# Optimization experiments

Measured on AMD Instinct MI355X. Metric: run time of the kernel, lower is better.

The kernel has to match this reference:

```python
import jax, jax.numpy as jnp
import numpy as np

B, CIN, COUT, T = 64, 2048, 2048, 128
BLOCK = 8            # structured-sparsity block size from _create_structured_sparse_mask
SPARSITY = 0.9       # keep probability per block = 1 - SPARSITY
SPIKE_PROB = 0.1     # binary input spike rate


def setup_inputs() -> dict:
    key = jax.random.key(0)
    k1, k2, k3 = jax.random.split(key, 3)
    # binary input spikes [B, Cin, T] (torch casts to int8; values are 0/1)
    spikes = (jax.random.uniform(k1, (B, CIN, T)) < SPIKE_PROB).astype(jnp.float32)
    # int8 quantized weights held as float32 (values in [-127,127))
    weights = jax.random.randint(k2, (COUT, CIN), -127, 127).astype(jnp.float32)
    # block-structured sparse connectivity mask, block 8x8, keep prob 0.1
    keep = jax.random.uniform(k3, (COUT // BLOCK, CIN // BLOCK)) > SPARSITY
    mask = jnp.repeat(jnp.repeat(keep, BLOCK, axis=0), BLOCK, axis=1).astype(jnp.float32)
    scale_exp = jnp.zeros((COUT,), dtype=jnp.int32)  # weight_scale_exp init zeros
    return {"spikes": spikes, "weights": weights, "mask": mask,
            "scale_exp": scale_exp, "threshold_exp": 7}


def reference(spikes, weights, mask, scale_exp, threshold_exp):
    # spikes: [B, Cin, T]; weights/mask: [Cout, Cin]; scale_exp: [Cout]
    masked_w = weights * mask                              # [Cout, Cin]
    scale = jnp.exp2(scale_exp.astype(jnp.float32))        # 2**weight_scale_exp per channel
    thr = jnp.float32(2.0) ** threshold_exp                # 2**threshold_exp (=128)
    s_t = jnp.transpose(spikes, (2, 0, 1))                 # [T, B, Cin]
    acc0 = jnp.zeros((spikes.shape[0], weights.shape[0]), jnp.float32)

    def step(acc, st):
        # integrate: sparse-masked matmul + power-of-two per-channel scale
        acc = acc + (st @ masked_w.T) * scale              # [B, Cout]
        spk = (acc >= thr).astype(jnp.float32)             # fire
        acc = acc * (1.0 - spk)                            # reset fired neurons to 0
        return acc, spk

    _, out = jax.lax.scan(step, acc0, s_t)                 # out: [T, B, Cout]
    return jnp.transpose(out, (1, 2, 0))                   # [B, Cout, T]
```

## Files before the change

kernel.cpp:

```cpp
#include <hip/hip_runtime.h>

#define BB   64
#define CIN  2048
#define COUT 2048
#define TT   128

#define NPAIR 64
#define NWIN  4
#define SLOTW 32
#define BC_CAP 7680

typedef int i32x4 __attribute__((ext_vector_type(4)));

__device__ __forceinline__ void async16(char* lds_dst, const char* g_src) {
    __builtin_amdgcn_global_load_lds(
        (const __attribute__((address_space(1))) void*)g_src,
        (__attribute__((address_space(3))) void*)lds_dst,
        16, 0, 0);
}

__global__ void prep1(const float* __restrict__ spikes,
                      const float* __restrict__ msk,
                      char* __restrict__ A,
                      unsigned long long* __restrict__ kb) {
    int bid = blockIdx.x;
    int tid = threadIdx.x;

    if (bid >= 8192) {
        int rb = bid - 8192;
        bool keep = (msk[(size_t)(rb * 8) * CIN + tid * 8] != 0.f);
        unsigned long long m = __ballot(keep);
        if ((tid & 63) == 0) kb[rb * 4 + (tid >> 6)] = m;
        return;
    }

    __shared__ float tile[64][33];
    int cc = bid & 31;
    int tt = (bid >> 5) & 3;
    int b  = bid >> 7;
    int c0 = cc * 64, t0 = tt * 32;

    int t4 = tid & 7;
    int cr = tid >> 3;
#pragma unroll
    for (int s = 0; s < 2; ++s) {
        int c = cr + s * 32;
        float4 v = *(const float4*)(spikes + ((size_t)b * CIN + c0 + c) * TT + t0 + t4 * 4);
        tile[c][t4 * 4 + 0] = v.x;
        tile[c][t4 * 4 + 1] = v.y;
        tile[c][t4 * 4 + 2] = v.z;
        tile[c][t4 * 4 + 3] = v.w;
    }
    __syncthreads();

    int tw_ = tid >> 4;
    int cq  = tid & 15;
#pragma unroll
    for (int s2 = 0; s2 < 2; ++s2) {
        int tw = tw_ + s2 * 16;
        int packed = 0;
#pragma unroll
        for (int q = 0; q < 4; ++q)
            packed |= ((tile[cq * 4 + q][tw] != 0.f) ? 1 : 0) << (8 * q);
        *(int*)(A + ((size_t)(b * TT) + t0 + tw) * CIN + c0 + cq * 4) = packed;
    }
}

__global__ void prep2(const float* __restrict__ w,
                      const float* __restrict__ msk,
                      const unsigned long long* __restrict__ kb,
                      char* __restrict__ Bc,
                      unsigned short* __restrict__ lst,
                      unsigned* __restrict__ ofs_g,
                      unsigned* __restrict__ nch_g) {
    __shared__ unsigned sbm[256];
    __shared__ unsigned snch[256];
    __shared__ unsigned sofs[256];
    const int tid = threadIdx.x;
    const int pw_self = blockIdx.x;

    {
        int p = tid >> 2, wdw = tid & 3;
        unsigned long long r = kb[(4 * p + 0) * 4 + wdw] | kb[(4 * p + 1) * 4 + wdw] |
                               kb[(4 * p + 2) * 4 + wdw] | kb[(4 * p + 3) * 4 + wdw];
        unsigned long long t2 = r | (r >> 1);
        unsigned bm = 0u;
#pragma unroll
        for (int s = 0; s < 32; ++s)
            bm |= (unsigned)((t2 >> (2 * s)) & 1ull) << s;
        sbm[tid]  = bm;
        snch[tid] = (unsigned)((__popc(bm) + 3) >> 2);
    }
    __syncthreads();
    if (tid == 0) {
        unsigned run = 0;
#pragma unroll 4
        for (int i = 0; i < 256; ++i) { sofs[i] = run; run += snch[i] * 4; }
        ofs_g[pw_self] = sofs[pw_self];
        nch_g[pw_self] = snch[pw_self];
    }
    __syncthreads();

    const int p = pw_self >> 2, wdw = pw_self & 3;
    unsigned rem = sbm[pw_self];
    const unsigned o = sofs[pw_self];
    const unsigned nslots = snch[pw_self] * 4;

    for (unsigned j = 0; j < nslots; ++j) {
        int kl = 0;
        bool real = false;
        if (rem) { kl = __ffs(rem) - 1; rem &= rem - 1u; real = true; }
        int kk = wdw * SLOTW + kl;
        if (tid < 128) {
            int col = tid >> 2, q = tid & 3;
            unsigned pk = 0u;
            if (real) {
                size_t base = (size_t)(p * 32 + col) * CIN + kk * 16 + q * 4;
                float4 a = *(const float4*)(w + base);
                float4 m = *(const float4*)(msk + base);
                int b0 = (int)(char)(int)(a.x * m.x);
                int b1 = (int)(char)(int)(a.y * m.y);
                int b2 = (int)(char)(int)(a.z * m.z);
                int b3 = (int)(char)(int)(a.w * m.w);
                pk = (unsigned)((b0 & 0xFF) | ((b1 & 0xFF) << 8) | ((b2 & 0xFF) << 16) | (b3 << 24));
            }
            *(unsigned*)(Bc + (size_t)(o + j) * 512 + col * 16 + q * 4) = pk;
        }
        if (tid == 0) lst[o + j] = (unsigned short)(real ? kl : 0);
    }
}

__global__ void __launch_bounds__(512, 4)
snn_gemm_scan(const char* __restrict__ A,
              const char* __restrict__ Bc,
              const unsigned short* __restrict__ lst,
              const unsigned* __restrict__ ofs,
              const unsigned* __restrict__ nchv,
              const int* __restrict__ scale_exp,
              const int* __restrict__ thr_exp,
              float* __restrict__ out) {
    __shared__ __align__(16) union {
        struct {
            char a[128 * 512];
            unsigned short l[8 * SLOTW];
            unsigned meta[16];
        } s;
        float c[128 * 132];
    } lds;
    __shared__ unsigned pb[128 * 4];

    const int tid  = threadIdx.x;
    const int lane = tid & 63;
    const int w    = tid >> 6;
    const int wr   = w >> 2;
    const int wp   = w & 3;

    const int bid = blockIdx.x;
    const int b  = bid & 63;
    const int nt = bid >> 6;
    const int m0 = b * TT;
    const int p0 = nt * 8;

    const int mrow = lane & 15, kc = lane >> 4;

    i32x4 acc[4][2][2] = {};

    for (int wdw = 0; wdw < NWIN; ++wdw) {
        __syncthreads();
        if (tid < 16) {
            int pl = tid >> 1;
            const unsigned* src = (tid & 1) ? nchv : ofs;
            lds.s.meta[tid] = src[(p0 + pl) * 4 + wdw];
        }
        if (tid < 128) {
            int pl = tid >> 4, e2 = tid & 15;
            unsigned o = ofs[(p0 + pl) * 4 + wdw];
            *(unsigned*)&lds.s.l[pl * SLOTW + e2 * 2] =
                *(const unsigned*)(lst + o + e2 * 2);
        }
#pragma unroll
        for (int i = 0; i < 8; ++i) {
            int f = i * 512 + tid;
            int row = f >> 5, g0 = f & 31;
            int src = (g0 & ~7) | ((g0 & 7) ^ (row & 7));
            async16((char*)lds.s.a + (size_t)f * 16,
                    A + (size_t)(m0 + row) * CIN + wdw * 512 + src * 16);
        }
        __syncthreads();

#pragma unroll
        for (int pi = 0; pi < 2; ++pi) {
            const int pl = wp * 2 + pi;
            const unsigned o   = lds.s.meta[pl * 2];
            const unsigned nch = lds.s.meta[pl * 2 + 1];
            const unsigned short* Lp = &lds.s.l[pl * SLOTW];
            for (unsigned c = 0; c < nch; ++c) {
                const int kk = (int)Lp[c * 4 + kc];
                const char* bp = Bc + (size_t)(o + c * 4 + kc) * 512 + mrow * 16;
                i32x4 bv0 = *(const i32x4*)bp;
                i32x4 bv1 = *(const i32x4*)(bp + 256);
#pragma unroll
                for (int mf = 0; mf < 4; ++mf) {
                    int row = wr * 64 + mf * 16 + mrow;
                    i32x4 av = *(const i32x4*)((const char*)lds.s.a +
                                  row * 512 + ((kk ^ (row & 7)) << 4));
                    acc[mf][pi][0] = __builtin_amdgcn_mfma_i32_16x16x64_i8(
                        av, bv0, acc[mf][pi][0], 0, 0, 0);
                    acc[mf][pi][1] = __builtin_amdgcn_mfma_i32_16x16x64_i8(
                        av, bv1, acc[mf][pi][1], 0, 0, 0);
                }
            }
        }
    }

    const float thr = exp2f((float)thr_exp[0]);
#pragma unroll
    for (int P = 0; P < 2; ++P) {
        __syncthreads();
        if ((wp >> 1) == P) {
            const int rb = (lane >> 4) * 4;
            const int cb = lane & 15;
            const int cbase = (wp & 1) * 64;
#pragma unroll
            for (int mf = 0; mf < 4; ++mf)
#pragma unroll
                for (int pi = 0; pi < 2; ++pi)
#pragma unroll
                    for (int cf = 0; cf < 2; ++cf)
#pragma unroll
                        for (int r = 0; r < 4; ++r)
                            lds.c[(wr * 64 + mf * 16 + rb + r) * 132 +
                                  cbase + pi * 32 + cf * 16 + cb] =
                                (float)acc[mf][pi][cf][r];
        }
        __syncthreads();

        if (tid < 128) {
            const float scale = exp2f((float)scale_exp[nt * 256 + P * 128 + tid]);
            float a = 0.f;
#pragma unroll
            for (int q = 0; q < 4; ++q) {
                unsigned bq = 0u;
#pragma unroll 8
                for (int j = 0; j < 32; ++j) {
                    a += lds.c[(q * 32 + j) * 132 + tid] * scale;
                    unsigned sp = (a >= thr) ? 1u : 0u;
                    if (sp) a = 0.f;
                    bq |= sp << j;
                }
                pb[tid * 4 + q] = bq;
            }
        }
        __syncthreads();

        const int t4 = tid & 31, u = tid >> 5;
#pragma unroll
        for (int s2 = 0; s2 < 8; ++s2) {
            int co = s2 * 16 + u;
            unsigned wb  = pb[co * 4 + (t4 >> 3)];
            unsigned nib = (wb >> ((t4 & 7) * 4)) & 0xFu;
            float4 v;
            v.x = (float)(nib & 1u);
            v.y = (float)((nib >> 1) & 1u);
            v.z = (float)((nib >> 2) & 1u);
            v.w = (float)((nib >> 3) & 1u);
            *(float4*)(out + (size_t)(b * COUT + nt * 256 + P * 128 + co) * TT
                       + t4 * 4) = v;
        }
    }
}

extern "C" void kernel_launch(void* const* d_in, const int* in_sizes, int n_in,
                              void* d_out, int out_size, void* d_ws, size_t ws_size,
                              hipStream_t stream) {
    const float* spikes  = (const float*)d_in[0];
    const float* weights = (const float*)d_in[1];
    const float* mask    = (const float*)d_in[2];
    const int*   scale_e = (const int*)d_in[3];
    const int*   thr_e   = (const int*)d_in[4];
    float* out = (float*)d_out;

    char* ws = (char*)d_ws;
    char*               Ai8  = ws;
    char*               Bc   = ws + 16777216;
    unsigned short*     lstp = (unsigned short*)(ws + 20709376);
    unsigned*           ofsp = (unsigned*)(ws + 20725760);
    unsigned*           nchp = (unsigned*)(ws + 20726784);
    unsigned long long* kbp  = (unsigned long long*)(ws + 20727808);

    prep1<<<BB * 4 * 32 + 256, 256, 0, stream>>>(spikes, mask, Ai8, kbp);
    prep2<<<NPAIR * NWIN, 256, 0, stream>>>(weights, mask, kbp, Bc, lstp, ofsp, nchp);
    snn_gemm_scan<<<8 * BB, 512, 0, stream>>>(Ai8, Bc, lstp, ofsp, nchp,
                                              scale_e, thr_e, out);
}
```

Before: 204.3 us.

## Retile spike transpose, preload sparse metadata once, prefetch B fragments in GEMM loop

```diff
diff --git a/kernel.cpp b/kernel.cpp
--- a/kernel.cpp
+++ b/kernel.cpp
@@ -8,7 +8,6 @@
 #define NPAIR 64
 #define NWIN  4
 #define SLOTW 32
-#define BC_CAP 7680
 
 typedef int i32x4 __attribute__((ext_vector_type(4)));
 
@@ -26,43 +25,39 @@
     int bid = blockIdx.x;
     int tid = threadIdx.x;
 
-    if (bid >= 8192) {
-        int rb = bid - 8192;
+    if (bid >= 2048) {
+        int rb = bid - 2048;
         bool keep = (msk[(size_t)(rb * 8) * CIN + tid * 8] != 0.f);
         unsigned long long m = __ballot(keep);
         if ((tid & 63) == 0) kb[rb * 4 + (tid >> 6)] = m;
         return;
     }
 
-    __shared__ float tile[64][33];
-    int cc = bid & 31;
-    int tt = (bid >> 5) & 3;
-    int b  = bid >> 7;
-    int c0 = cc * 64, t0 = tt * 32;
-
-    int t4 = tid & 7;
-    int cr = tid >> 3;
-#pragma unroll
-    for (int s = 0; s < 2; ++s) {
-        int c = cr + s * 32;
-        float4 v = *(const float4*)(spikes + ((size_t)b * CIN + c0 + c) * TT + t0 + t4 * 4);
-        tile[c][t4 * 4 + 0] = v.x;
-        tile[c][t4 * 4 + 1] = v.y;
-        tile[c][t4 * 4 + 2] = v.z;
-        tile[c][t4 * 4 + 3] = v.w;
+    __shared__ float tile[32][256];
+    int cg = bid & 7, tg = (bid >> 3) & 3, b = bid >> 5;
+    int c0 = cg * 256, t0 = tg * 32;
+
+    {
+        const float* src = spikes + ((size_t)b * CIN + c0 + tid) * TT + t0;
+#pragma unroll
+        for (int j = 0; j < 8; ++j) {
+            float4 v = *(const float4*)(src + j * 4);
+            tile[j * 4 + 0][tid] = v.x;
+            tile[j * 4 + 1][tid] = v.y;
+            tile[j * 4 + 2][tid] = v.z;
+            tile[j * 4 + 3][tid] = v.w;
+        }
     }
     __syncthreads();
 
-    int tw_ = tid >> 4;
-    int cq  = tid & 15;
-#pragma unroll
-    for (int s2 = 0; s2 < 2; ++s2) {
-        int tw = tw_ + s2 * 16;
-        int packed = 0;
-#pragma unroll
-        for (int q = 0; q < 4; ++q)
-            packed |= ((tile[cq * 4 + q][tw] != 0.f) ? 1 : 0) << (8 * q);
-        *(int*)(A + ((size_t)(b * TT) + t0 + tw) * CIN + c0 + cq * 4) = packed;
+    const int cq = tid & 63, tw = tid >> 6;
+#pragma unroll
+    for (int s2 = 0; s2 < 8; ++s2) {
+        int t = s2 * 4 + tw;
+        float4 v = *(const float4*)&tile[t][cq * 4];
+        unsigned pk = (v.x != 0.f ? 0x1u : 0u) | (v.y != 0.f ? 0x100u : 0u) |
+                      (v.z != 0.f ? 0x10000u : 0u) | (v.w != 0.f ? 0x1000000u : 0u);
+        *(unsigned*)(A + ((size_t)(b * TT) + t0 + t) * CIN + c0 + cq * 4) = pk;
     }
 }
 
@@ -140,13 +135,12 @@
               const int* __restrict__ thr_exp,
               float* __restrict__ out) {
     __shared__ __align__(16) union {
-        struct {
-            char a[128 * 512];
-            unsigned short l[8 * SLOTW];
-            unsigned meta[16];
-        } s;
+        char a[128 * 512];
         float c[128 * 132];
     } lds;
+    __shared__ unsigned short slist[8][NWIN][SLOTW];
+    __shared__ unsigned smeta_ofs[32];
+    __shared__ unsigned smeta_nch[32];
     __shared__ unsigned pb[128 * 4];
 
     const int tid  = threadIdx.x;
@@ -163,27 +157,31 @@
 
     const int mrow = lane & 15, kc = lane >> 4;
 
+    if (tid < 64) {
+        int i = tid & 31;
+        unsigned g = (p0 + (i >> 2)) * 4 + (i & 3);
+        if (tid < 32) smeta_ofs[i] = ofs[g];
+        else          smeta_nch[i] = nchv[g];
+    }
+    {
+        int pl = tid >> 6;
+        int rest = tid & 63;
+        int w2 = rest >> 4, e = (rest & 15) * 2;
+        unsigned g = (p0 + pl) * 4 + w2;
+        unsigned o = ofs[g];
+        *(unsigned*)&slist[pl][w2][e] = *(const unsigned*)(lst + o + e);
+    }
+
     i32x4 acc[4][2][2] = {};
 
     for (int wdw = 0; wdw < NWIN; ++wdw) {
         __syncthreads();
-        if (tid < 16) {
-            int pl = tid >> 1;
-            const unsigned* src = (tid & 1) ? nchv : ofs;
-            lds.s.meta[tid] = src[(p0 + pl) * 4 + wdw];
-        }
-        if (tid < 128) {
-            int pl = tid >> 4, e2 = tid & 15;
-            unsigned o = ofs[(p0 + pl) * 4 + wdw];
-            *(unsigned*)&lds.s.l[pl * SLOTW + e2 * 2] =
-                *(const unsigned*)(lst + o + e2 * 2);
-        }
 #pragma unroll
         for (int i = 0; i < 8; ++i) {
             int f = i * 512 + tid;
             int row = f >> 5, g0 = f & 31;
             int src = (g0 & ~7) | ((g0 & 7) ^ (row & 7));
-            async16((char*)lds.s.a + (size_t)f * 16,
+            async16((char*)lds.a + (size_t)f * 16,
                     A + (size_t)(m0 + row) * CIN + wdw * 512 + src * 16);
         }
         __syncthreads();
@@ -191,23 +189,37 @@
 #pragma unroll
         for (int pi = 0; pi < 2; ++pi) {
             const int pl = wp * 2 + pi;
-            const unsigned o   = lds.s.meta[pl * 2];
-            const unsigned nch = lds.s.meta[pl * 2 + 1];
-            const unsigned short* Lp = &lds.s.l[pl * SLOTW];
+            const unsigned o   = smeta_ofs[pl * 4 + wdw];
+            const unsigned nch = smeta_nch[pl * 4 + wdw];
+            const unsigned short* Lp = &slist[pl][wdw][0];
+            if (nch == 0) continue;
+            const char* bbase = Bc + (size_t)o * 512 + mrow * 16 + (size_t)kc * 512;
+
+            int   kkN = (int)Lp[kc];
+            i32x4 b0N = *(const i32x4*)bbase;
             for (unsigned c = 0; c < nch; ++c) {
-                const int kk = (int)Lp[c * 4 + kc];
-                const char* bp = Bc + (size_t)(o + c * 4 + kc) * 512 + mrow * 16;
-                i32x4 bv0 = *(const i32x4*)bp;
-                i32x4 bv1 = *(const i32x4*)(bp + 256);
+                const int   kkC = kkN;
+                const i32x4 b0C = b0N;
+                i32x4 b1C = *(const i32x4*)(bbase + (size_t)c * 2048 + 256);
+                if (c + 1 < nch) {
+                    kkN = (int)Lp[(c + 1) * 4 + kc];
+                    b0N = *(const i32x4*)(bbase + (size_t)(c + 1) * 2048);
+                }
 #pragma unroll
                 for (int mf = 0; mf < 4; ++mf) {
                     int row = wr * 64 + mf * 16 + mrow;
-                    i32x4 av = *(const i32x4*)((const char*)lds.s.a +
-                                  row * 512 + ((kk ^ (row & 7)) << 4));
+                    i32x4 av = *(const i32x4*)((const char*)lds.a +
+                                  row * 512 + ((kkC ^ (row & 7)) << 4));
                     acc[mf][pi][0] = __builtin_amdgcn_mfma_i32_16x16x64_i8(
-                        av, bv0, acc[mf][pi][0], 0, 0, 0);
+                        av, b0C, acc[mf][pi][0], 0, 0, 0);
+                }
+#pragma unroll
+                for (int mf = 0; mf < 4; ++mf) {
+                    int row = wr * 64 + mf * 16 + mrow;
+                    i32x4 av = *(const i32x4*)((const char*)lds.a +
+                                  row * 512 + ((kkC ^ (row & 7)) << 4));
                     acc[mf][pi][1] = __builtin_amdgcn_mfma_i32_16x16x64_i8(
-                        av, bv1, acc[mf][pi][1], 0, 0, 0);
+                        av, b1C, acc[mf][pi][1], 0, 0, 0);
                 }
             }
         }
@@ -288,7 +300,7 @@
     unsigned*           nchp = (unsigned*)(ws + 20726784);
     unsigned long long* kbp  = (unsigned long long*)(ws + 20727808);
 
-    prep1<<<BB * 4 * 32 + 256, 256, 0, stream>>>(spikes, mask, Ai8, kbp);
+    prep1<<<2048 + 256, 256, 0, stream>>>(spikes, mask, Ai8, kbp);
     prep2<<<NPAIR * NWIN, 256, 0, stream>>>(weights, mask, kbp, Bc, lstp, ofsp, nchp);
     snn_gemm_scan<<<8 * BB, 512, 0, stream>>>(Ai8, Bc, lstp, ofsp, nchp,
                                               scale_e, thr_e, out);
```

Measured after the change: 222.1 us. 1.09x slower.
